# Kernel tuning notes

Hardware: AMD Instinct MI355X
Metric: run time of the kernel (lower is better)

The kernel has to match this reference:

```python
import jax, jax.numpy as jnp
import numpy as np

NUM_FRAMES = 36
NUM_QUERIES = 36000            # num_out = 1000
NUM_TGT = 256                  # flat targets = NUM_TGT * NUM_FRAMES = 9216
NUM_CLASSES = 81
COST_CLASS = 1.0
COST_BBOX = 1.0
COST_GIOU = 1.0


def box_cxcywh_to_xyxy(b):
    cx, cy, w, h = b[..., 0], b[..., 1], b[..., 2], b[..., 3]
    return jnp.stack([cx - 0.5 * w, cy - 0.5 * h, cx + 0.5 * w, cy + 0.5 * h], axis=-1)


def multi_giou(a, b):
    # elementwise (broadcasted) generalized IoU over last-dim xyxy boxes
    lt = jnp.maximum(a[..., :2], b[..., :2])
    rb = jnp.minimum(a[..., 2:], b[..., 2:])
    wh = jnp.clip(rb - lt, 0.0)
    inter = wh[..., 0] * wh[..., 1]
    area_a = (a[..., 2] - a[..., 0]) * (a[..., 3] - a[..., 1])
    area_b = (b[..., 2] - b[..., 0]) * (b[..., 3] - b[..., 1])
    union = area_a + area_b - inter
    iou = inter / union
    lt_c = jnp.minimum(a[..., :2], b[..., :2])
    rb_c = jnp.maximum(a[..., 2:], b[..., 2:])
    wh_c = jnp.clip(rb_c - lt_c, 0.0)
    area_c = wh_c[..., 0] * wh_c[..., 1]
    return iou - (area_c - union) / area_c


def setup_inputs() -> dict:
    key = jax.random.key(0)
    k1, k2, k3, k4 = jax.random.split(key, 4)
    pred_logits = jax.random.normal(k1, (NUM_QUERIES, NUM_CLASSES), dtype=jnp.float32)
    pred_boxes = jax.random.uniform(k2, (NUM_QUERIES, 4), dtype=jnp.float32,
                                    minval=0.05, maxval=0.95)
    tgt_bbox = jax.random.uniform(k3, (NUM_TGT * NUM_FRAMES, 4), dtype=jnp.float32,
                                  minval=0.05, maxval=0.95)
    tgt_ids = jax.random.randint(k4, (NUM_TGT * NUM_FRAMES,), 0, NUM_CLASSES)
    return {
        "pred_logits": pred_logits,
        "pred_boxes": pred_boxes,
        "tgt_bbox": tgt_bbox,
        "tgt_ids": tgt_ids,
        "num_frames": NUM_FRAMES,
    }


def reference(pred_logits, pred_boxes, tgt_bbox, tgt_ids, num_frames):
    Q, C = pred_logits.shape
    F = num_frames
    O = Q // F                      # num_out (queries per frame / tracks)
    T = tgt_ids.shape[0] // F       # num targets (tracks)

    out_prob = jax.nn.softmax(pred_logits, axis=-1)
    # [F, O, C] -> [O, F, C]
    out_prob_split = jnp.transpose(out_prob.reshape(F, O, C), (1, 0, 2))
    # gather over (frame, class) pairs: frame_index repeats 0..F-1 per target
    frame_index = jnp.tile(jnp.arange(F), T)          # [T*F]
    class_cost = -out_prob_split[:, frame_index, tgt_ids]      # [O, T*F]
    class_cost = class_cost.reshape(O, T, F).mean(axis=-1)     # [O, T]

    # [O, 1, F, 4] vs [1, T, F, 4]
    out_bbox_split = jnp.transpose(pred_boxes.reshape(F, O, 4), (1, 0, 2))[:, None]
    tgt_bbox_split = tgt_bbox.reshape(T, F, 4)[None]
    bbox_cost = jnp.abs(out_bbox_split - tgt_bbox_split).mean(axis=(-1, -2))  # [O, T]

    giou = multi_giou(box_cxcywh_to_xyxy(out_bbox_split),
                      box_cxcywh_to_xyxy(tgt_bbox_split))       # [O, T, F]
    iou_cost = -giou.mean(axis=-1)                              # [O, T]

    cost = COST_CLASS * class_cost + COST_BBOX * bbox_cost + COST_GIOU * iou_cost
    return cost
```

## Files before the change

kernel.cpp:

```cpp
#include <hip/hip_runtime.h>
#include <hip/hip_bf16.h>

#define NF 36
#define NO 1000
#define NT 256
#define NC 81

__global__ __launch_bounds__(256) void matcher_fused_kernel(
    const float* __restrict__ logits,
    const float* __restrict__ pboxes,
    const float* __restrict__ tboxes,
    const int*   __restrict__ tids,
    float* __restrict__ out)
{
    const int o    = blockIdx.x;
    const int tid  = threadIdx.x;
    const int wave = tid >> 6;
    const int lane = tid & 63;

    __shared__ float        prob[NF * NC];
    __shared__ unsigned int ids_w[NT * NF / 4];
    __shared__ float4       pbx[NF];
    __shared__ float        pbarea[NF];

    {
        const int4* src = (const int4*)tids;
        #pragma unroll
        for (int i = tid; i < NT * NF / 4; i += 256) {
            const int4 v = src[i];
            ids_w[i] = (unsigned int)(v.x & 0xff)
                     | ((unsigned int)(v.y & 0xff) << 8)
                     | ((unsigned int)(v.z & 0xff) << 16)
                     | ((unsigned int)(v.w & 0xff) << 24);
        }
    }

    if (tid < NF) {
        const float4 pc = ((const float4*)pboxes)[tid * NO + o];
        float4 x;
        x.x = pc.x - 0.5f * pc.z;  x.y = pc.y - 0.5f * pc.w;
        x.z = pc.x + 0.5f * pc.z;  x.w = pc.y + 0.5f * pc.w;
        pbx[tid] = x;
        pbarea[tid] = pc.z * pc.w;
    }

    for (int f = wave; f < NF; f += 4) {
        const float* row = logits + (size_t)(f * NO + o) * NC;
        float e1 = (lane      < NC) ? __expf(row[lane])      : 0.0f;
        float e2 = (lane + 64 < NC) ? __expf(row[lane + 64]) : 0.0f;
        float s = e1 + e2;
        #pragma unroll
        for (int m = 32; m; m >>= 1) s += __shfl_xor(s, m);
        const float inv = __builtin_amdgcn_rcpf(s);
        if (lane      < NC) prob[f * NC + lane]      = e1 * inv;
        if (lane + 64 < NC) prob[f * NC + lane + 64] = e2 * inv;
    }
    __syncthreads();

    const int t = tid;
    const float4* __restrict__ tb4 = (const float4*)tboxes;
    const unsigned char* __restrict__ ids8 = (const unsigned char*)ids_w;

    float acc_cls = 0.0f, acc_l1 = 0.0f, acc_giou = 0.0f;

    #pragma unroll 3
    for (int g = 0; g < NF / 4; ++g) {
        float4 tb[4];
        #pragma unroll
        for (int j = 0; j < 4; ++j) tb[j] = tb4[t * NF + g * 4 + j];

        #pragma unroll
        for (int j = 0; j < 4; ++j) {
            const int f = g * 4 + j;
            const float4 b = tb[j];
            const float4 pb = pbx[f];

            acc_cls += prob[f * NC + ids8[t * NF + f]];

            const float bx0 = b.x - 0.5f * b.z, by0 = b.y - 0.5f * b.w;
            const float bx1 = b.x + 0.5f * b.z, by1 = b.y + 0.5f * b.w;

            acc_l1 += fabsf(pb.x - bx0) + fabsf(pb.y - by0)
                    + fabsf(pb.z - bx1) + fabsf(pb.w - by1)
                    ;

            const float ltx = fmaxf(pb.x, bx0), lty = fmaxf(pb.y, by0);
            const float rbx = fminf(pb.z, bx1), rby = fminf(pb.w, by1);
            const float inter = fmaxf(rbx - ltx, 0.0f) * fmaxf(rby - lty, 0.0f);

            const float uni = pbarea[f] + b.z * b.w - inter;

            const float cx0 = fminf(pb.x, bx0), cy0 = fminf(pb.y, by0);
            const float cx1 = fmaxf(pb.z, bx1), cy1 = fmaxf(pb.w, by1);
            const float area_c = (cx1 - cx0) * (cy1 - cy0);

            acc_giou += inter * __builtin_amdgcn_rcpf(uni)
                      - (area_c - uni) * __builtin_amdgcn_rcpf(area_c);
        }
    }

    acc_l1 = 0.0f;
    #pragma unroll 3
    for (int g = 0; g < NF / 4; ++g) {
        float4 tb[4];
        #pragma unroll
        for (int j = 0; j < 4; ++j) tb[j] = tb4[t * NF + g * 4 + j];
        #pragma unroll
        for (int j = 0; j < 4; ++j) {
            const int f = g * 4 + j;
            const float4 b = tb[j];
            const float4 pb = pbx[f];
            const float pcx = 0.5f * (pb.x + pb.z), pcy = 0.5f * (pb.y + pb.w);
            const float pw  = pb.z - pb.x,          ph  = pb.w - pb.y;
            acc_l1 += fabsf(pcx - b.x) + fabsf(pcy - b.y)
                    + fabsf(pw  - b.z) + fabsf(ph  - b.w);
        }
    }

    const float inv_f  = 1.0f / (float)NF;
    const float inv_4f = 1.0f / (float)(4 * NF);
    out[(size_t)o * NT + t] = -(acc_cls + acc_giou) * inv_f + acc_l1 * inv_4f;
}

extern "C" void kernel_launch(void* const* d_in, const int* in_sizes, int n_in,
                              void* d_out, int out_size, void* d_ws, size_t ws_size,
                              hipStream_t stream) {
    const float* pred_logits = (const float*)d_in[0];
    const float* pred_boxes  = (const float*)d_in[1];
    const float* tgt_bbox    = (const float*)d_in[2];
    const int*   tgt_ids     = (const int*)d_in[3];
    float* out = (float*)d_out;
    (void)d_ws; (void)ws_size;

    matcher_fused_kernel<<<NO, 256, 0, stream>>>(
        pred_logits, pred_boxes, tgt_bbox, tgt_ids, out);
}
```

Measured before the change: 94.43 us.

## Fuse L1 pass into GIoU loop, read ids directly, batch logit loads

Removes the second pass over target boxes by computing the L1 cost in cxcywh form inside the main GIoU loop, using a cached copy of the predicted cxcywh boxes in shared memory. Drops the per-block packing of all 9216 target ids into shared memory and reads ids as int4 straight from global memory in the main loop. Issues all nine logit row loads per wave before the exp/softmax work to raise memory-level parallelism, and adds a min-blocks launch bound. The batched loads and launch bound raise register pressure, and the ids are now read from global per thread instead of once per block.

```diff
diff --git a/kernel.cpp b/kernel.cpp
--- a/kernel.cpp
+++ b/kernel.cpp
@@ -6,7 +6,7 @@
 #define NT 256
 #define NC 81
 
-__global__ __launch_bounds__(256) void matcher_fused_kernel(
+__global__ __launch_bounds__(256, 4) void matcher_fused2_kernel(
     const float* __restrict__ logits,
     const float* __restrict__ pboxes,
     const float* __restrict__ tboxes,
@@ -18,102 +18,81 @@
     const int wave = tid >> 6;
     const int lane = tid & 63;
 
-    __shared__ float        prob[NF * NC];
-    __shared__ unsigned int ids_w[NT * NF / 4];
-    __shared__ float4       pbx[NF];
-    __shared__ float        pbarea[NF];
+    __shared__ float  prob[NF * NC];
+    __shared__ float4 pbc[NF];
+    __shared__ float4 pbx[NF];
 
-    {
-        const int4* src = (const int4*)tids;
-        #pragma unroll
-        for (int i = tid; i < NT * NF / 4; i += 256) {
-            const int4 v = src[i];
-            ids_w[i] = (unsigned int)(v.x & 0xff)
-                     | ((unsigned int)(v.y & 0xff) << 8)
-                     | ((unsigned int)(v.z & 0xff) << 16)
-                     | ((unsigned int)(v.w & 0xff) << 24);
-        }
+    float x1[9], x2[9];
+    #pragma unroll
+    for (int k = 0; k < 9; ++k) {
+        const int f = wave + 4 * k;
+        const float* row = logits + (size_t)(f * NO + o) * NC;
+        x1[k] = (lane      < NC) ? row[lane]      : 0.0f;
+        x2[k] = (lane + 64 < NC) ? row[lane + 64] : 0.0f;
     }
-
     if (tid < NF) {
         const float4 pc = ((const float4*)pboxes)[tid * NO + o];
+        pbc[tid] = pc;
         float4 x;
         x.x = pc.x - 0.5f * pc.z;  x.y = pc.y - 0.5f * pc.w;
         x.z = pc.x + 0.5f * pc.z;  x.w = pc.y + 0.5f * pc.w;
         pbx[tid] = x;
-        pbarea[tid] = pc.z * pc.w;
     }
 
-    for (int f = wave; f < NF; f += 4) {
-        const float* row = logits + (size_t)(f * NO + o) * NC;
-        float e1 = (lane      < NC) ? __expf(row[lane])      : 0.0f;
-        float e2 = (lane + 64 < NC) ? __expf(row[lane + 64]) : 0.0f;
-        float s = e1 + e2;
+    #pragma unroll
+    for (int k = 0; k < 9; ++k) {
+        const int f = wave + 4 * k;
+        const float a = (lane      < NC) ? __expf(x1[k]) : 0.0f;
+        const float b = (lane + 64 < NC) ? __expf(x2[k]) : 0.0f;
+        float s = a + b;
         #pragma unroll
         for (int m = 32; m; m >>= 1) s += __shfl_xor(s, m);
         const float inv = __builtin_amdgcn_rcpf(s);
-        if (lane      < NC) prob[f * NC + lane]      = e1 * inv;
-        if (lane + 64 < NC) prob[f * NC + lane + 64] = e2 * inv;
+        if (lane      < NC) prob[f * NC + lane]      = a * inv;
+        if (lane + 64 < NC) prob[f * NC + lane + 64] = b * inv;
     }
     __syncthreads();
 
     const int t = tid;
     const float4* __restrict__ tb4 = (const float4*)tboxes;
-    const unsigned char* __restrict__ ids8 = (const unsigned char*)ids_w;
 
     float acc_cls = 0.0f, acc_l1 = 0.0f, acc_giou = 0.0f;
 
     #pragma unroll 3
     for (int g = 0; g < NF / 4; ++g) {
+        const int4 c4 = *(const int4*)(tids + t * NF + g * 4);
         float4 tb[4];
         #pragma unroll
         for (int j = 0; j < 4; ++j) tb[j] = tb4[t * NF + g * 4 + j];
+        const int cls[4] = {c4.x, c4.y, c4.z, c4.w};
 
         #pragma unroll
         for (int j = 0; j < 4; ++j) {
             const int f = g * 4 + j;
-            const float4 b = tb[j];
-            const float4 pb = pbx[f];
+            const float4 b  = tb[j];
+            const float4 qc = pbc[f];
+            const float4 qx = pbx[f];
 
-            acc_cls += prob[f * NC + ids8[t * NF + f]];
+            acc_cls += prob[f * NC + cls[j]];
+
+            acc_l1 += fabsf(qc.x - b.x) + fabsf(qc.y - b.y)
+                    + fabsf(qc.z - b.z) + fabsf(qc.w - b.w);
 
             const float bx0 = b.x - 0.5f * b.z, by0 = b.y - 0.5f * b.w;
             const float bx1 = b.x + 0.5f * b.z, by1 = b.y + 0.5f * b.w;
 
-            acc_l1 += fabsf(pb.x - bx0) + fabsf(pb.y - by0)
-                    + fabsf(pb.z - bx1) + fabsf(pb.w - by1)
-                    ;
-
-            const float ltx = fmaxf(pb.x, bx0), lty = fmaxf(pb.y, by0);
-            const float rbx = fminf(pb.z, bx1), rby = fminf(pb.w, by1);
+            const float ltx = fmaxf(qx.x, bx0), lty = fmaxf(qx.y, by0);
+            const float rbx = fminf(qx.z, bx1), rby = fminf(qx.w, by1);
             const float inter = fmaxf(rbx - ltx, 0.0f) * fmaxf(rby - lty, 0.0f);
 
-            const float uni = pbarea[f] + b.z * b.w - inter;
+            const float uni = qc.z * qc.w + b.z * b.w - inter;
 
-            const float cx0 = fminf(pb.x, bx0), cy0 = fminf(pb.y, by0);
-            const float cx1 = fmaxf(pb.z, bx1), cy1 = fmaxf(pb.w, by1);
+            const float cx0 = fminf(qx.x, bx0), cy0 = fminf(qx.y, by0);
+            const float cx1 = fmaxf(qx.z, bx1), cy1 = fmaxf(qx.w, by1);
             const float area_c = (cx1 - cx0) * (cy1 - cy0);
 
             acc_giou += inter * __builtin_amdgcn_rcpf(uni)
                       - (area_c - uni) * __builtin_amdgcn_rcpf(area_c);
-        }
-    }
-
-    acc_l1 = 0.0f;
-    #pragma unroll 3
-    for (int g = 0; g < NF / 4; ++g) {
-        float4 tb[4];
-        #pragma unroll
-        for (int j = 0; j < 4; ++j) tb[j] = tb4[t * NF + g * 4 + j];
-        #pragma unroll
-        for (int j = 0; j < 4; ++j) {
-            const int f = g * 4 + j;
-            const float4 b = tb[j];
-            const float4 pb = pbx[f];
-            const float pcx = 0.5f * (pb.x + pb.z), pcy = 0.5f * (pb.y + pb.w);
-            const float pw  = pb.z - pb.x,          ph  = pb.w - pb.y;
-            acc_l1 += fabsf(pcx - b.x) + fabsf(pcy - b.y)
-                    + fabsf(pw  - b.z) + fabsf(ph  - b.w);
         }
     }
 
@@ -132,6 +111,6 @@
     float* out = (float*)d_out;
     (void)d_ws; (void)ws_size;
 
-    matcher_fused_kernel<<<NO, 256, 0, stream>>>(
+    matcher_fused2_kernel<<<NO, 256, 0, stream>>>(
         pred_logits, pred_boxes, tgt_bbox, tgt_ids, out);
 }
```

Result: faster. 87.16 us (-7.7%).
